# Kernel optimization log

Hardware: AMD Instinct MI355X
Metric: run time of the kernel (lower is better)

## Reference

```python
import jax, jax.numpy as jnp
import numpy as np

NC = 128      # nc
K = 5         # cube kernel size
NS = 3        # n_scale pyramid levels
NV = 150000   # vertices (cortical-surface scale)
NF = 300000   # faces ~ 2*NV
L = 192       # volume side (L = W = H -> rescale = [1,1,1])


def setup_inputs() -> dict:
    key = jax.random.key(0)
    ks = jax.random.split(key, 16)
    s = 0.05
    return {
        "v": jax.random.uniform(ks[0], (1, NV, 3), minval=-0.9, maxval=0.9, dtype=jnp.float32),
        "f": jax.random.randint(ks[1], (1, NF, 3), 0, NV, dtype=jnp.int32),
        "volume": jax.random.normal(ks[2], (1, 1, L, L, L), dtype=jnp.float32),
        "fc1_w": jax.random.normal(ks[3], (6, NC), dtype=jnp.float32) * s,
        "fc1_b": jnp.zeros((NC,), jnp.float32),
        "fc2_w": jax.random.normal(ks[4], (2 * NC, 4 * NC), dtype=jnp.float32) * s,
        "fc2_b": jnp.zeros((4 * NC,), jnp.float32),
        "fc3_w": jax.random.normal(ks[5], (4 * NC, 2 * NC), dtype=jnp.float32) * s,
        "fc3_b": jnp.zeros((2 * NC,), jnp.float32),
        "fc4_w": jax.random.normal(ks[6], (2 * NC, 3), dtype=jnp.float32) * s,
        "fc4_b": jnp.zeros((3,), jnp.float32),
        "conv_w": jax.random.normal(ks[7], (NC, NS, K, K, K), dtype=jnp.float32) * s,
        "conv_b": jnp.zeros((NC,), jnp.float32),
        "lfc_w": jax.random.normal(ks[8], (NC, NC), dtype=jnp.float32) * s,
        "lfc_b": jnp.zeros((NC,), jnp.float32),
    }


def _vertex_normals(v, f):
    # pytorch3d-style vertex normals: scatter-add area-weighted face normals, then normalize.
    verts, faces = v[0], f[0]
    p0, p1, p2 = verts[faces[:, 0]], verts[faces[:, 1]], verts[faces[:, 2]]
    fn = jnp.cross(p1 - p0, p2 - p0)  # [NF, 3]
    n = jnp.zeros_like(verts)
    n = n.at[faces[:, 0]].add(fn).at[faces[:, 1]].add(fn).at[faces[:, 2]].add(fn)
    n = n / jnp.maximum(jnp.linalg.norm(n, axis=-1, keepdims=True), 1e-12)
    return n[None]  # [1, NV, 3]


def _cube_sampling(v, volume):
    # Vectorized version of the 125-iteration Python gather loop:
    # gather a KxKxK neighborhood per vertex at each pyramid scale.
    vol_n = volume[0, 0]
    off = jnp.arange(-(K - 1) // 2, (K - 1) // 2 + 1)  # [-2..2]
    cubes = []
    for n in range(NS):
        if n > 0:
            s = vol_n.shape[0]
            vol_n = vol_n.reshape(s // 2, 2, s // 2, 2, s // 2, 2).mean(axis=(1, 3, 5))  # avg_pool3d(2)
        idx = jnp.round((v[0] + 1.0) * L / 2 ** (n + 1)).astype(jnp.int32)  # rescale = [1,1,1]
        idx = jnp.clip(idx, (K - 1) // 2, L // 2 ** n - 3)
        i0 = idx[:, 0, None, None, None] + off[None, :, None, None]
        i1 = idx[:, 1, None, None, None] + off[None, None, :, None]
        i2 = idx[:, 2, None, None, None] + off[None, None, None, :]
        cubes.append(vol_n[i0, i1, i2])  # [NV, K, K, K]
    return jnp.stack(cubes, axis=1)  # [NV, NS, K, K, K]


def reference(v, f, volume, fc1_w, fc1_b, fc2_w, fc2_b, fc3_w, fc3_b, fc4_w, fc4_b,
              conv_w, conv_b, lfc_w, lfc_b):
    coord = v
    normal = _vertex_normals(v, f)
    x = jnp.concatenate([v, normal], axis=2)                 # [1, NV, 6]
    x = jax.nn.leaky_relu(x @ fc1_w + fc1_b, 0.15)           # [1, NV, NC]
    cubes = _cube_sampling(v, volume)                        # [NV, NS, K, K, K]
    # Conv3d with kernel == input size -> single output voxel == full contraction.
    x_local = jnp.einsum('ncijk,ocijk->no', cubes, conv_w) + conv_b  # [NV, NC]
    x_local = (x_local @ lfc_w + lfc_b)[None]                # [1, NV, NC]
    x = jnp.concatenate([x, x_local], axis=2)                # [1, NV, 2*NC]
    x = jax.nn.leaky_relu(x @ fc2_w + fc2_b, 0.15)
    x = jax.nn.leaky_relu(x @ fc3_w + fc3_b, 0.15)
    x = jnp.tanh(x @ fc4_w + fc4_b) * 0.1
    return coord + x
```

## Files before the change

kernel.cpp:

```cpp
#include <hip/hip_runtime.h>
#include <hip/hip_bf16.h>
#include <math.h>

#define NVERT 150000
#define NFACE 300000
#define LVOL  192
#define TVB   32
#define MTV   48

#define P2_POOL1 3456
#define P2_POOL2 432
#define P2_WC    193
#define P2_CP0   3456
#define P2_POOL2_START (P2_POOL1)
#define P2_WC_START    (P2_POOL1 + P2_POOL2)
#define P2_CP0_START   (P2_POOL1 + P2_POOL2 + P2_WC)

#define NB_NORM 1172
#define NB_TRS  1024

#define NBUCKET 13824
#define WS_BIG_NEED  44808576ull
#define WS_B16_NEED  58964352ull
#define WS_SORT_NEED 60219648ull

typedef short v8s __attribute__((ext_vector_type(8)));
typedef float v4f __attribute__((ext_vector_type(4)));

__device__ __forceinline__ float s2f(short s) {
    unsigned int u = ((unsigned int)(unsigned short)s) << 16;
    return __builtin_bit_cast(float, u);
}
__device__ __forceinline__ short f2s(float f) {
    __hip_bfloat16 h = __float2bfloat16(f);
    return __builtin_bit_cast(short, h);
}
__device__ __forceinline__ float lrelu(float x) { return x > 0.f ? x : 0.15f * x; }

__device__ __forceinline__ float ldf(const void* __restrict__ p, int i, int bf) {
    return bf ? s2f(((const short*)p)[i]) : ((const float*)p)[i];
}

__device__ __forceinline__ int haddr(int r, int c) {
    int hi  = c >> 7;
    int mid = (c >> 4) & 7;
    int lo  = c & 15;
    int wc  = hi * 64 + (mid & 3) * 16 + lo;
    return ((mid < 4) ? 0 : 12672) + r * 264 + wc;
}

__global__ void detect_kernel(const void* __restrict__ v, int* __restrict__ flag) {
    __shared__ int s_ok;
    int t = threadIdx.x;
    if (t == 0) s_ok = 1;
    __syncthreads();
    float x = s2f(((const short*)v)[t]);
    if (!(fabsf(x) <= 1.0f)) atomicAnd(&s_ok, 0);
    __syncthreads();
    if (t == 0) *flag = s_ok;
}

__global__ __launch_bounds__(256) void sort_hist_kernel(
    const void* __restrict__ v, int* __restrict__ hist, int* __restrict__ keys,
    const int* __restrict__ flag)
{
    const int bf = *flag;
    int vert = blockIdx.x * 256 + threadIdx.x;
    if (vert >= NVERT) return;
    float vx = ldf(v, vert * 3 + 0, bf);
    float vy = ldf(v, vert * 3 + 1, bf);
    float vz = ldf(v, vert * 3 + 2, bf);
    int cx = min(max((int)rintf((vx + 1.0f) * 96.0f), 2), 189);
    int cy = min(max((int)rintf((vy + 1.0f) * 96.0f), 2), 189);
    int cz = min(max((int)rintf((vz + 1.0f) * 96.0f), 2), 189);
    int key = ((cx >> 3) * 24 + (cy >> 3)) * 24 + (cz >> 3);
    keys[vert] = key;
    atomicAdd(&hist[key], 1);
}

__global__ __launch_bounds__(1024) void sort_scan_kernel(int* __restrict__ hist)
{
    __shared__ int partial[1024];
    const int t = threadIdx.x;
    const int CH = 14;
    int base = t * CH;
    int sum = 0;
    #pragma unroll
    for (int i = 0; i < CH; i++) {
        int idx = base + i;
        if (idx < NBUCKET) sum += hist[idx];
    }
    partial[t] = sum;
    __syncthreads();
    for (int off = 1; off < 1024; off <<= 1) {
        int x = (t >= off) ? partial[t - off] : 0;
        __syncthreads();
        partial[t] += x;
        __syncthreads();
    }
    int run = partial[t] - sum;
    for (int i = 0; i < CH; i++) {
        int idx = base + i;
        if (idx < NBUCKET) {
            int c = hist[idx];
            hist[idx] = run;
            run += c;
        }
    }
}

__global__ __launch_bounds__(256) void sort_scatter_kernel(
    int* __restrict__ cursor, const int* __restrict__ keys, int* __restrict__ perm)
{
    int vert = blockIdx.x * 256 + threadIdx.x;
    if (vert >= NVERT) return;
    int pos = atomicAdd(&cursor[keys[vert]], 1);
    perm[pos] = vert;
}

__global__ __launch_bounds__(256) void mega_prep2_kernel(
    const void* __restrict__ volume,
    short* __restrict__ vol1b, short* __restrict__ vol2b,
    const void* __restrict__ conv_w, const void* __restrict__ lfc_w,
    const void* __restrict__ conv_b, const void* __restrict__ lfc_b,
    short* __restrict__ Wcomb, float* __restrict__ bcomb,
    const int* __restrict__ flag,
    short* __restrict__ vol0b)
{
    const int bf = *flag;
    const int bid = blockIdx.x;
    const int t = threadIdx.x;

    if (bid < P2_POOL1) {
        int id = bid * 256 + t;
        int z = id % 96, y = (id / 96) % 96, x = id / (96 * 96);
        float s = 0.f;
        #pragma unroll
        for (int a = 0; a < 2; a++)
            #pragma unroll
            for (int b = 0; b < 2; b++)
                #pragma unroll
                for (int c = 0; c < 2; c++)
                    s += ldf(volume, (2 * x + a) * (LVOL * LVOL) + (2 * y + b) * LVOL + (2 * z + c), bf);
        s *= 0.125f;
        vol1b[id] = f2s(s);
    } else if (bid < P2_WC_START) {
        int id = (bid - P2_POOL2_START) * 256 + t;
        int z = id % 48, y = (id / 48) % 48, x = id / (48 * 48);
        float s = 0.f;
        for (int a = 0; a < 4; a++)
            for (int b = 0; b < 4; b++)
                #pragma unroll
                for (int c = 0; c < 4; c++)
                    s += ldf(volume, (4 * x + a) * (LVOL * LVOL) + (4 * y + b) * LVOL + (4 * z + c), bf);
        s *= 0.015625f;
        vol2b[id] = f2s(s);
    } else if (bid < P2_CP0_START) {
        int id = (bid - P2_WC_START) * 256 + t;
        if (id < 49152) {
            int j = id / 384, k = id - j * 384;
            float acc = 0.f;
            if (k < 375) {
                float a0 = 0.f, a1 = 0.f, a2 = 0.f, a3 = 0.f;
                for (int o = 0; o < 128; o += 4) {
                    a0 += ldf(conv_w, (o + 0) * 375 + k, bf) * ldf(lfc_w, (o + 0) * 128 + j, bf);
                    a1 += ldf(conv_w, (o + 1) * 375 + k, bf) * ldf(lfc_w, (o + 1) * 128 + j, bf);
                    a2 += ldf(conv_w, (o + 2) * 375 + k, bf) * ldf(lfc_w, (o + 2) * 128 + j, bf);
                    a3 += ldf(conv_w, (o + 3) * 375 + k, bf) * ldf(lfc_w, (o + 3) * 128 + j, bf);
                }
                acc = (a0 + a1) + (a2 + a3);
            }
            int tile = j >> 4, ln = j & 15;
            int kk = k >> 5, r = k & 31, qq = r >> 3, e = r & 7;
            Wcomb[((tile * 12 + kk) * 64 + qq * 16 + ln) * 8 + e] = f2s(acc);
        } else if (id < 49152 + 128) {
            int j = id - 49152;
            float acc = ldf(lfc_b, j, bf);
            for (int o = 0; o < 128; o++) acc += ldf(conv_b, o, bf) * ldf(lfc_w, o * 128 + j, bf);
            bcomb[j] = acc;
        }
    } else {
        if (bf) return;
        int id = (bid - P2_CP0_START) * 2048 + t * 8;
        const float* vp = (const float*)volume;
        short tmp[8];
        #pragma unroll
        for (int i = 0; i < 8; i++) tmp[i] = f2s(vp[id + i]);
        *(v8s*)&vol0b[id] = *(v8s*)tmp;
    }
}

__global__ __launch_bounds__(256, 6) void gather_ext_kernel(
    const void* __restrict__ v,
    const int* __restrict__ f, float* __restrict__ n_accum,
    const void* __restrict__ volume,
    const short* __restrict__ vol1b,
    const short* __restrict__ vol2b,
    const short* __restrict__ vol0b,
    const int* __restrict__ perm,
    const short* __restrict__ Wcomb,
    const float* __restrict__ bcomb,
    const void* __restrict__ fc2_w, const void* __restrict__ fc3_w,
    short* __restrict__ fc2T, short* __restrict__ fc3T,
    short* __restrict__ xloc,
    const int* __restrict__ flag, int ngather)
{
    __shared__ __align__(16) short sCube[TVB * 392];
    __shared__ int sIdx[TVB * 4];

    const int bf = *flag;
    const int t = threadIdx.x;
    const int bid = blockIdx.x;

    if (bid >= ngather) {
        int rb = bid - ngather;
        if (rb < NB_NORM) {
            int ft = rb * 256 + t;
            if (ft >= NFACE) return;
            int i0 = f[ft * 3 + 0], i1 = f[ft * 3 + 1], i2 = f[ft * 3 + 2];
            float p0x = ldf(v, i0 * 3 + 0, bf), p0y = ldf(v, i0 * 3 + 1, bf), p0z = ldf(v, i0 * 3 + 2, bf);
            float p1x = ldf(v, i1 * 3 + 0, bf), p1y = ldf(v, i1 * 3 + 1, bf), p1z = ldf(v, i1 * 3 + 2, bf);
            float p2x = ldf(v, i2 * 3 + 0, bf), p2y = ldf(v, i2 * 3 + 1, bf), p2z = ldf(v, i2 * 3 + 2, bf);
            float e1x = p1x - p0x, e1y = p1y - p0y, e1z = p1z - p0z;
            float e2x = p2x - p0x, e2y = p2y - p0y, e2z = p2z - p0z;
            float cx = e1y * e2z - e1z * e2y;
            float cy = e1z * e2x - e1x * e2z;
            float cz = e1x * e2y - e1y * e2x;
            atomicAdd(&n_accum[i0 * 3 + 0], cx); atomicAdd(&n_accum[i0 * 3 + 1], cy); atomicAdd(&n_accum[i0 * 3 + 2], cz);
            atomicAdd(&n_accum[i1 * 3 + 0], cx); atomicAdd(&n_accum[i1 * 3 + 1], cy); atomicAdd(&n_accum[i1 * 3 + 2], cz);
            atomicAdd(&n_accum[i2 * 3 + 0], cx); atomicAdd(&n_accum[i2 * 3 + 1], cy); atomicAdd(&n_accum[i2 * 3 + 2], cz);
        } else {
            int id = (rb - NB_NORM) * 256 + t;
            if (id < 131072) {
                int col = id >> 8, k = id & 255;
                int tile = col >> 4, ln = col & 15;
                int kk = k >> 5, r = k & 31, qq = r >> 3, e = r & 7;
                fc2T[((tile * 8 + kk) * 64 + qq * 16 + ln) * 8 + e] = f2s(ldf(fc2_w, k * 512 + col, bf));
            } else {
                int i = id - 131072;
                int col = i >> 9, k = i & 511;
                int tile = col >> 4, ln = col & 15;
                int kk = k >> 5, r = k & 31, qq = r >> 3, e = r & 7;
                fc3T[((tile * 16 + kk) * 64 + qq * 16 + ln) * 8 + e] = f2s(ldf(fc3_w, k * 256 + col, bf));
            }
        }
        return;
    }

    const int base = bid * TVB;
    const int w = t >> 6, L = t & 63, q = L >> 4, ln = L & 15;
    const short* v0 = bf ? (const short*)volume : vol0b;

    if (t < TVB) {
        int slot = min(base + t, NVERT - 1);
        int vert = perm ? perm[slot] : slot;
        float vx = ldf(v, vert * 3 + 0, bf);
        float vy = ldf(v, vert * 3 + 1, bf);
        float vz = ldf(v, vert * 3 + 2, bf);
        #pragma unroll
        for (int n = 0; n < 3; n++) {
            float scl = (n == 0) ? 96.0f : (n == 1 ? 48.0f : 24.0f);
            int dim = LVOL >> n, lim = dim - 3;
            int cx = min(max((int)rintf((vx + 1.0f) * scl), 2), lim);
            int cy = min(max((int)rintf((vy + 1.0f) * scl), 2), lim);
            int cz = min(max((int)rintf((vz + 1.0f) * scl), 2), lim);
            sIdx[t * 4 + n] = (cx * dim + cy) * dim + (cz - 2);
        }
    }
    __syncthreads();

    for (int idx = t; idx < TVB * 75; idx += 256) {
        int n   = idx / 800;
        int rem = idx - n * 800;
        int vl  = rem / 25;
        int dd  = rem - vl * 25;
        int di  = dd / 5, dj = dd - di * 5;
        int dim = LVOL >> n;
        int addr = sIdx[vl * 4 + n] + (di - 2) * dim * dim + (dj - 2) * dim;
        short* dst = &sCube[vl * 392 + n * 125 + dd * 5];
        if (n == 0 && v0 == nullptr) {
            const float* vp = (const float*)volume;
            #pragma unroll
            for (int i = 0; i < 5; i++) dst[i] = f2s(vp[addr + i]);
        } else {
            const short* lvl = (n == 0) ? v0 : (n == 1 ? vol1b : vol2b);
            #pragma unroll
            for (int i = 0; i < 5; i++) dst[i] = lvl[addr + i];
        }
    }
    for (int idx = t; idx < TVB * 9; idx += 256) {
        int vl = idx / 9, rr = idx - vl * 9;
        sCube[vl * 392 + 375 + rr] = 0;
    }
    __syncthreads();

    #pragma unroll
    for (int nt = 0; nt < 2; nt++) {
        int col = w * 32 + nt * 16 + ln;
        const short* wb = Wcomb + ((w * 2 + nt) * 12 * 64 + q * 16 + ln) * 8;
        v4f acc0 = {0.f, 0.f, 0.f, 0.f}, acc1 = {0.f, 0.f, 0.f, 0.f};
        #pragma unroll
        for (int k0 = 0; k0 < 12; k0++) {
            v8s b  = *(const v8s*)(wb + k0 * 512);
            v8s a0 = *(const v8s*)&sCube[ln * 392 + k0 * 32 + q * 8];
            v8s a1 = *(const v8s*)&sCube[(16 + ln) * 392 + k0 * 32 + q * 8];
            acc0 = __builtin_amdgcn_mfma_f32_16x16x32_bf16(a0, b, acc0, 0, 0, 0);
            acc1 = __builtin_amdgcn_mfma_f32_16x16x32_bf16(a1, b, acc1, 0, 0, 0);
        }
        float bias = bcomb[col];
        #pragma unroll
        for (int r = 0; r < 4; r++) {
            xloc[(base + q * 4 + r) * 128 + col]      = f2s(acc0[r] + bias);
            xloc[(base + 16 + q * 4 + r) * 128 + col] = f2s(acc1[r] + bias);
        }
    }
}

__global__ __launch_bounds__(256, 3) void mlp_kernel(
    const void* __restrict__ v,
    const float* __restrict__ n_accum,
    const short* __restrict__ xloc,
    const int* __restrict__ perm,
    const short* __restrict__ fc2T,
    const short* __restrict__ fc3T,
    const void* __restrict__ fc1_w, const void* __restrict__ fc1_b,
    const void* __restrict__ fc2_b, const void* __restrict__ fc3_b,
    const void* __restrict__ fc4_w, const void* __restrict__ fc4_b,
    void* __restrict__ out,
    const int* __restrict__ flag)
{
    __shared__ __align__(16) char smem[52224];
    short* sX  = (short*)smem;
    short* sHB = (short*)smem;
    short* s3  = (short*)smem;
    short* sW4 = (short*)(smem + 50688);

    const int bf = *flag;
    const int t = threadIdx.x;
    const int base = blockIdx.x * MTV;
    const int w = t >> 6, L = t & 63, q = L >> 4, ln = L & 15;
    const int laneoff = (q * 16 + ln) * 8;

    for (int id = t; id < MTV * 16; id += 256) {
        int row = id >> 4, seg = id & 15;
        v8s x = *(const v8s*)(xloc + (base + row) * 128 + seg * 8);
        *(v8s*)&sX[row * 264 + 128 + seg * 8] = x;
    }

    for (int i = t; i < 768; i += 256) {
        int j = i >> 8, k = i & 255;
        sW4[i] = f2s(ldf(fc4_w, k * 3 + j, bf));
    }

    {
        int vi = t >> 2, cb = (t & 3) * 32;
        if (vi < MTV) {
            int vert = perm ? perm[base + vi] : (base + vi);
            float i0 = ldf(v, vert * 3 + 0, bf);
            float i1 = ldf(v, vert * 3 + 1, bf);
            float i2 = ldf(v, vert * 3 + 2, bf);
            float nx = n_accum[vert * 3 + 0];
            float ny = n_accum[vert * 3 + 1];
            float nz = n_accum[vert * 3 + 2];
            float inv = 1.0f / fmaxf(sqrtf(nx * nx + ny * ny + nz * nz), 1e-12f);
            float i3 = nx * inv, i4 = ny * inv, i5 = nz * inv;
            #pragma unroll 8
            for (int i = 0; i < 32; i++) {
                int c = cb + i;
                float acc = ldf(fc1_b, c, bf)
                          + i0 * ldf(fc1_w, 0 * 128 + c, bf)
                          + i1 * ldf(fc1_w, 1 * 128 + c, bf)
                          + i2 * ldf(fc1_w, 2 * 128 + c, bf)
                          + i3 * ldf(fc1_w, 3 * 128 + c, bf)
                          + i4 * ldf(fc1_w, 4 * 128 + c, bf)
                          + i5 * ldf(fc1_w, 5 * 128 + c, bf);
                sX[vi * 264 + c] = f2s(lrelu(acc));
            }
        }
    }
    __syncthreads();

    {
        #pragma unroll
        for (int nt = 4; nt < 8; nt++) {
            int col = w * 128 + nt * 16 + ln;
            const short* bb = fc2T + (w * 8 + nt) * 8 * 512 + laneoff;
            v4f acc0 = {0.f, 0.f, 0.f, 0.f}, acc1 = {0.f, 0.f, 0.f, 0.f}, acc2 = {0.f, 0.f, 0.f, 0.f};
            #pragma unroll
            for (int k0 = 0; k0 < 8; k0++) {
                v8s b  = *(const v8s*)(bb + k0 * 512);
                v8s a0 = *(const v8s*)&sX[(ln) * 264 + k0 * 32 + q * 8];
                v8s a1 = *(const v8s*)&sX[(16 + ln) * 264 + k0 * 32 + q * 8];
                v8s a2 = *(const v8s*)&sX[(32 + ln) * 264 + k0 * 32 + q * 8];
                acc0 = __builtin_amdgcn_mfma_f32_16x16x32_bf16(a0, b, acc0, 0, 0, 0);
                acc1 = __builtin_amdgcn_mfma_f32_16x16x32_bf16(a1, b, acc1, 0, 0, 0);
                acc2 = __builtin_amdgcn_mfma_f32_16x16x32_bf16(a2, b, acc2, 0, 0, 0);
            }
            float bias = ldf(fc2_b, col, bf);
            int wc = 12672 + w * 64 + (nt - 4) * 16 + ln;
            #pragma unroll
            for (int r = 0; r < 4; r++) {
                sHB[(q * 4 + r) * 264 + wc]      = f2s(lrelu(acc0[r] + bias));
                sHB[(16 + q * 4 + r) * 264 + wc] = f2s(lrelu(acc1[r] + bias));
                sHB[(32 + q * 4 + r) * 264 + wc] = f2s(lrelu(acc2[r] + bias));
            }
        }

        v4f accL[4][3];
        #pragma unroll
        for (int nt = 0; nt < 4; nt++)
            #pragma unroll
            for (int m = 0; m < 3; m++)
                accL[nt][m] = (v4f){0.f, 0.f, 0.f, 0.f};

        #pragma unroll
        for (int nt = 0; nt < 4; nt++) {
            const short* bb = fc2T + (w * 8 + nt) * 8 * 512 + laneoff;
            #pragma unroll
            for (int k0 = 0; k0 < 8; k0++) {
                v8s b  = *(const v8s*)(bb + k0 * 512);
                v8s a0 = *(const v8s*)&sX[(ln) * 264 + k0 * 32 + q * 8];
                v8s a1 = *(const v8s*)&sX[(16 + ln) * 264 + k0 * 32 + q * 8];
                v8s a2 = *(const v8s*)&sX[(32 + ln) * 264 + k0 * 32 + q * 8];
                accL[nt][0] = __builtin_amdgcn_mfma_f32_16x16x32_bf16(a0, b, accL[nt][0], 0, 0, 0);
                accL[nt][1] = __builtin_amdgcn_mfma_f32_16x16x32_bf16(a1, b, accL[nt][1], 0, 0, 0);
                accL[nt][2] = __builtin_amdgcn_mfma_f32_16x16x32_bf16(a2, b, accL[nt][2], 0, 0, 0);
            }
        }
        __syncthreads();

        #pragma unroll
        for (int nt = 0; nt < 4; nt++) {
            int col = w * 128 + nt * 16 + ln;
            float bias = ldf(fc2_b, col, bf);
            int wc = w * 64 + nt * 16 + ln;
            #pragma unroll
            for (int r = 0; r < 4; r++) {
                sHB[(q * 4 + r) * 264 + wc]      = f2s(lrelu(accL[nt][0][r] + bias));
                sHB[(16 + q * 4 + r) * 264 + wc] = f2s(lrelu(accL[nt][1][r] + bias));
                sHB[(32 + q * 4 + r) * 264 + wc] = f2s(lrelu(accL[nt][2][r] + bias));
            }
        }
    }
    __syncthreads();

    {
        v4f acc[4][3];
        #pragma unroll
        for (int nt = 0; nt < 4; nt++)
            #pragma unroll
            for (int m = 0; m < 3; m++)
                acc[nt][m] = (v4f){0.f, 0.f, 0.f, 0.f};

        #pragma unroll
        for (int half = 0; half < 2; half++) {
            v8s A0[8], A1[8], A2[8];
            #pragma unroll
            for (int k0 = 0; k0 < 8; k0++) {
                int c = half * 256 + k0 * 32 + q * 8;
                A0[k0] = *(const v8s*)&sHB[haddr(ln, c)];
                A1[k0] = *(const v8s*)&sHB[haddr(16 + ln, c)];
                A2[k0] = *(const v8s*)&sHB[haddr(32 + ln, c)];
            }
            #pragma unroll
            for (int nt = 0; nt < 4; nt++) {
                const short* bb = fc3T + ((w * 4 + nt) * 16 + half * 8) * 512 + laneoff;
                v8s B[8];
                #pragma unroll
                for (int k0 = 0; k0 < 8; k0++) B[k0] = *(const v8s*)(bb + k0 * 512);
                #pragma unroll
                for (int k0 = 0; k0 < 8; k0++) {
                    acc[nt][0] = __builtin_amdgcn_mfma_f32_16x16x32_bf16(A0[k0], B[k0], acc[nt][0], 0, 0, 0);
                    acc[nt][1] = __builtin_amdgcn_mfma_f32_16x16x32_bf16(A1[k0], B[k0], acc[nt][1], 0, 0, 0);
                    acc[nt][2] = __builtin_amdgcn_mfma_f32_16x16x32_bf16(A2[k0], B[k0], acc[nt][2], 0, 0, 0);
                }
            }
        }
        __syncthreads();

        #pragma unroll
        for (int nt = 0; nt < 4; nt++) {
            int col = w * 64 + nt * 16 + ln;
            float bias = ldf(fc3_b, col, bf);
            #pragma unroll
            for (int r = 0; r < 4; r++) {
                s3[(q * 4 + r) * 264 + col]      = f2s(lrelu(acc[nt][0][r] + bias));
                s3[(16 + q * 4 + r) * 264 + col] = f2s(lrelu(acc[nt][1][r] + bias));
                s3[(32 + q * 4 + r) * 264 + col] = f2s(lrelu(acc[nt][2][r] + bias));
            }
        }
    }
    __syncthreads();

    {
        int vi = t >> 2, l = t & 3;
        if (vi < MTV) {
            float p0 = 0.f, p1 = 0.f, p2 = 0.f;
            for (int k = l * 8; k < 256; k += 32) {
                #pragma unroll
                for (int j = 0; j < 8; j++) {
                    float a = s2f(s3[vi * 264 + k + j]);
                    p0 += a * s2f(sW4[0 * 256 + k + j]);
                    p1 += a * s2f(sW4[1 * 256 + k + j]);
                    p2 += a * s2f(sW4[2 * 256 + k + j]);
                }
            }
            #pragma unroll
            for (int s = 2; s; s >>= 1) {
                p0 += __shfl_down(p0, s, 4);
                p1 += __shfl_down(p1, s, 4);
                p2 += __shfl_down(p2, s, 4);
            }
            if (l == 0) {
                int vert = perm ? perm[base + vi] : (base + vi);
                float vx = ldf(v, vert * 3 + 0, bf);
                float vy = ldf(v, vert * 3 + 1, bf);
                float vz = ldf(v, vert * 3 + 2, bf);
                float o0 = vx + 0.1f * tanhf(p0 + ldf(fc4_b, 0, bf));
                float o1 = vy + 0.1f * tanhf(p1 + ldf(fc4_b, 1, bf));
                float o2 = vz + 0.1f * tanhf(p2 + ldf(fc4_b, 2, bf));
                if (bf) {
                    short* ob = (short*)out;
                    ob[vert * 3 + 0] = f2s(o0);
                    ob[vert * 3 + 1] = f2s(o1);
                    ob[vert * 3 + 2] = f2s(o2);
                } else {
                    float* of = (float*)out;
                    of[vert * 3 + 0] = o0;
                    of[vert * 3 + 1] = o1;
                    of[vert * 3 + 2] = o2;
                }
            }
        }
    }
}

__global__ __launch_bounds__(256, 3) void fused_mfma_kernel(
    const void* __restrict__ v,
    const float* __restrict__ n_accum,
    const void* __restrict__ volume,
    const short* __restrict__ vol1,
    const short* __restrict__ vol2,
    const short* __restrict__ Wcomb,
    const float* __restrict__ bcomb,
    const short* __restrict__ fc2T,
    const short* __restrict__ fc3T,
    const void* __restrict__ fc1_w, const void* __restrict__ fc1_b,
    const void* __restrict__ fc2_b, const void* __restrict__ fc3_b,
    const void* __restrict__ fc4_w, const void* __restrict__ fc4_b,
    void* __restrict__ out,
    const int* __restrict__ flag)
{
    __shared__ __align__(16) char smem[51712];
    short* sX    = (short*)smem;
    short* sCube = (short*)(smem + 16896);
    short* sH    = (short*)(smem + 16896);
    short* s3    = (short*)smem;
    short* sW4   = (short*)(smem + 50176);

    const int bf = *flag;
    const int t = threadIdx.x;
    const int base = blockIdx.x * TVB;
    const int w = t >> 6, L = t & 63, q = L >> 4, ln = L & 15;
    const int laneoff = (q * 16 + ln) * 8;

    for (int idx = t; idx < TVB * 75; idx += 256) {
        int vl  = idx / 75;
        int r75 = idx - vl * 75;
        int n   = r75 / 25;
        int dd  = r75 - n * 25;
        int di  = dd / 5, dj = dd - di * 5;
        int vert = base + vl;
        short* dst = &sCube[vl * 392 + n * 125 + dd * 5];
        if (vert < NVERT) {
            float vx = ldf(v, vert * 3 + 0, bf);
            float vy = ldf(v, vert * 3 + 1, bf);
            float vz = ldf(v, vert * 3 + 2, bf);
            float scl = (n == 0) ? 96.0f : (n == 1 ? 48.0f : 24.0f);
            int lim = (LVOL >> n) - 3;
            int cx = (int)rintf((vx + 1.0f) * scl);
            int cy = (int)rintf((vy + 1.0f) * scl);
            int cz = (int)rintf((vz + 1.0f) * scl);
            cx = min(max(cx, 2), lim) + di - 2;
            cy = min(max(cy, 2), lim) + dj - 2;
            cz = min(max(cz, 2), lim);
            if (n == 0) {
                int b0 = (cx * LVOL + cy) * LVOL + (cz - 2);
                if (bf) {
                    const short* vp = (const short*)volume;
                    #pragma unroll
                    for (int i = 0; i < 5; i++) dst[i] = vp[b0 + i];
                } else {
                    const float* vp = (const float*)volume;
                    #pragma unroll
                    for (int i = 0; i < 5; i++) dst[i] = f2s(vp[b0 + i]);
                }
            } else {
                const short* lvl = (n == 1) ? vol1 : vol2;
                int dim = (n == 1) ? 96 : 48;
                int b0 = (cx * dim + cy) * dim + (cz - 2);
                #pragma unroll
                for (int i = 0; i < 5; i++) dst[i] = lvl[b0 + i];
            }
        } else {
            #pragma unroll
            for (int i = 0; i < 5; i++) dst[i] = 0;
        }
    }
    for (int idx = t; idx < TVB * 9; idx += 256) {
        int vl = idx / 9, rr = idx - vl * 9;
        sCube[vl * 392 + 375 + rr] = 0;
    }
    for (int i = t; i < 768; i += 256) {
        int j = i >> 8, k = i & 255;
        sW4[i] = f2s(ldf(fc4_w, k * 3 + j, bf));
    }
    {
        int vi = t & 31, cb = (t >> 5) * 16;
        int vert = base + vi;
        float i0 = 0.f, i1 = 0.f, i2 = 0.f, i3 = 0.f, i4 = 0.f, i5 = 0.f;
        if (vert < NVERT) {
            i0 = ldf(v, vert * 3 + 0, bf);
            i1 = ldf(v, vert * 3 + 1, bf);
            i2 = ldf(v, vert * 3 + 2, bf);
            float nx = n_accum[vert * 3 + 0];
            float ny = n_accum[vert * 3 + 1];
            float nz = n_accum[vert * 3 + 2];
            float inv = 1.0f / fmaxf(sqrtf(nx * nx + ny * ny + nz * nz), 1e-12f);
            i3 = nx * inv; i4 = ny * inv; i5 = nz * inv;
        }
        #pragma unroll
        for (int i = 0; i < 16; i++) {
            int c = cb + i;
            float acc = ldf(fc1_b, c, bf)
                      + i0 * ldf(fc1_w, 0 * 128 + c, bf)
                      + i1 * ldf(fc1_w, 1 * 128 + c, bf)
                      + i2 * ldf(fc1_w, 2 * 128 + c, bf)
                      + i3 * ldf(fc1_w, 3 * 128 + c, bf)
                      + i4 * ldf(fc1_w, 4 * 128 + c, bf)
                      + i5 * ldf(fc1_w, 5 * 128 + c, bf);
            sX[vi * 264 + c] = f2s(lrelu(acc));
        }
    }
    __syncthreads();

    #pragma unroll
    for (int nt = 0; nt < 2; nt++) {
        int col = w * 32 + nt * 16 + ln;
        const short* wb = Wcomb + ((w * 2 + nt) * 12 * 64) * 8 + laneoff;
        v4f acc0 = {0.f, 0.f, 0.f, 0.f}, acc1 = {0.f, 0.f, 0.f, 0.f};
        #pragma unroll
        for (int k0 = 0; k0 < 12; k0++) {
            v8s b  = *(const v8s*)(wb + k0 * 512);
            v8s a0 = *(const v8s*)&sCube[ln * 392 + k0 * 32 + q * 8];
            v8s a1 = *(const v8s*)&sCube[(16 + ln) * 392 + k0 * 32 + q * 8];
            acc0 = __builtin_amdgcn_mfma_f32_16x16x32_bf16(a0, b, acc0, 0, 0, 0);
            acc1 = __builtin_amdgcn_mfma_f32_16x16x32_bf16(a1, b, acc1, 0, 0, 0);
        }
        float bias = bcomb[col];
        #pragma unroll
        for (int r = 0; r < 4; r++) {
            sX[(q * 4 + r) * 264 + 128 + col]      = f2s(acc0[r] + bias);
            sX[(16 + q * 4 + r) * 264 + 128 + col] = f2s(acc1[r] + bias);
        }
    }
    __syncthreads();

    {
        v8s a0[8], a1[8];
        #pragma unroll
        for (int k0 = 0; k0 < 8; k0++) {
            a0[k0] = *(const v8s*)&sX[ln * 264 + k0 * 32 + q * 8];
            a1[k0] = *(const v8s*)&sX[(16 + ln) * 264 + k0 * 32 + q * 8];
        }
        #pragma unroll
        for (int nt = 0; nt < 8; nt++) {
            int col = w * 128 + nt * 16 + ln;
            const short* bb = fc2T + (w * 8 + nt) * 8 * 512 + laneoff;
            v4f acc0 = {0.f, 0.f, 0.f, 0.f}, acc1 = {0.f, 0.f, 0.f, 0.f};
            #pragma unroll
            for (int k0 = 0; k0 < 8; k0++) {
                v8s b = *(const v8s*)(bb + k0 * 512);
                acc0 = __builtin_amdgcn_mfma_f32_16x16x32_bf16(a0[k0], b, acc0, 0, 0, 0);
                acc1 = __builtin_amdgcn_mfma_f32_16x16x32_bf16(a1[k0], b, acc1, 0, 0, 0);
            }
            float bias = ldf(fc2_b, col, bf);
            #pragma unroll
            for (int r = 0; r < 4; r++) {
                sH[(q * 4 + r) * 520 + col]      = f2s(lrelu(acc0[r] + bias));
                sH[(16 + q * 4 + r) * 520 + col] = f2s(lrelu(acc1[r] + bias));
            }
        }
    }
    __syncthreads();

    {
        #pragma unroll
        for (int nt = 0; nt < 4; nt++) {
            int col = w * 64 + nt * 16 + ln;
            v4f acc0 = {0.f, 0.f, 0.f, 0.f}, acc1 = {0.f, 0.f, 0.f, 0.f};
            #pragma unroll
            for (int half = 0; half < 2; half++) {
                const short* bb = fc3T + ((w * 4 + nt) * 16 + half * 8) * 512 + laneoff;
                #pragma unroll
                for (int k0 = 0; k0 < 8; k0++) {
                    v8s b  = *(const v8s*)(bb + k0 * 512);
                    v8s a0 = *(const v8s*)&sH[ln * 520 + half * 256 + k0 * 32 + q * 8];
                    v8s a1 = *(const v8s*)&sH[(16 + ln) * 520 + half * 256 + k0 * 32 + q * 8];
                    acc0 = __builtin_amdgcn_mfma_f32_16x16x32_bf16(a0, b, acc0, 0, 0, 0);
                    acc1 = __builtin_amdgcn_mfma_f32_16x16x32_bf16(a1, b, acc1, 0, 0, 0);
                }
            }
            float bias = ldf(fc3_b, col, bf);
            #pragma unroll
            for (int r = 0; r < 4; r++) {
                s3[(q * 4 + r) * 264 + col]      = f2s(lrelu(acc0[r] + bias));
                s3[(16 + q * 4 + r) * 264 + col] = f2s(lrelu(acc1[r] + bias));
            }
        }
    }
    __syncthreads();

    {
        int vi = t >> 3, l = t & 7;
        float p0 = 0.f, p1 = 0.f, p2 = 0.f;
        for (int k = l; k < 256; k += 8) {
            float a = s2f(s3[vi * 264 + k]);
            p0 += a * s2f(sW4[0 * 256 + k]);
            p1 += a * s2f(sW4[1 * 256 + k]);
            p2 += a * s2f(sW4[2 * 256 + k]);
        }
        #pragma unroll
        for (int s = 4; s; s >>= 1) {
            p0 += __shfl_down(p0, s, 8);
            p1 += __shfl_down(p1, s, 8);
            p2 += __shfl_down(p2, s, 8);
        }
        if (l == 0) {
            int vert = base + vi;
            if (vert < NVERT) {
                float vx = ldf(v, vert * 3 + 0, bf);
                float vy = ldf(v, vert * 3 + 1, bf);
                float vz = ldf(v, vert * 3 + 2, bf);
                float o0 = vx + 0.1f * tanhf(p0 + ldf(fc4_b, 0, bf));
                float o1 = vy + 0.1f * tanhf(p1 + ldf(fc4_b, 1, bf));
                float o2 = vz + 0.1f * tanhf(p2 + ldf(fc4_b, 2, bf));
                if (bf) {
                    short* ob = (short*)out;
                    ob[vert * 3 + 0] = f2s(o0);
                    ob[vert * 3 + 1] = f2s(o1);
                    ob[vert * 3 + 2] = f2s(o2);
                } else {
                    float* of = (float*)out;
                    of[vert * 3 + 0] = o0;
                    of[vert * 3 + 1] = o1;
                    of[vert * 3 + 2] = o2;
                }
            }
        }
    }
}

extern "C" void kernel_launch(void* const* d_in, const int* in_sizes, int n_in,
                              void* d_out, int out_size, void* d_ws, size_t ws_size,
                              hipStream_t stream) {
    const void* v      = d_in[0];
    const int*  f      = (const int*)d_in[1];
    const void* volume = d_in[2];
    const void* fc1_w  = d_in[3];
    const void* fc1_b  = d_in[4];
    const void* fc2_w  = d_in[5];
    const void* fc2_b  = d_in[6];
    const void* fc3_w  = d_in[7];
    const void* fc3_b  = d_in[8];
    const void* fc4_w  = d_in[9];
    const void* fc4_b  = d_in[10];
    const void* conv_w = d_in[11];
    const void* conv_b = d_in[12];
    const void* lfc_w  = d_in[13];
    const void* lfc_b  = d_in[14];

    char* wsb = (char*)d_ws;
    const int big  = (ws_size >= WS_BIG_NEED) ? 1 : 0;
    const int b16  = (ws_size >= WS_B16_NEED) ? 1 : 0;
    const int srt  = (ws_size >= WS_SORT_NEED) ? 1 : 0;

    if (big) {
        int*   flag    = (int*)wsb;
        float* n_accum = (float*)(wsb + 64);
        short* vol1b   = (short*)(wsb + 1800064);
        short* vol2b   = (short*)(wsb + 5339008);
        short* Wcomb   = (short*)(wsb + 5781376);
        float* bcomb   = (float*)(wsb + 5879680);
        short* fc2T    = (short*)(wsb + 5880192);
        short* fc3T    = (short*)(wsb + 6142336);
        short* xloc    = (short*)(wsb + 6404480);
        short* vol0b   = b16 ? (short*)(wsb + 44808576) : nullptr;
        int*   hist    = srt ? (int*)(wsb + 58964352) : nullptr;
        int*   keys    = srt ? (int*)(wsb + 59019648) : nullptr;
        int*   perm    = srt ? (int*)(wsb + 59619648) : nullptr;

        hipMemsetAsync(n_accum, 0, NVERT * 3 * sizeof(float), stream);
        detect_kernel<<<1, 256, 0, stream>>>(v, flag);
        if (srt) {
            hipMemsetAsync(hist, 0, NBUCKET * sizeof(int), stream);
            sort_hist_kernel<<<(NVERT + 255) / 256, 256, 0, stream>>>(v, hist, keys, flag);
            sort_scan_kernel<<<1, 1024, 0, stream>>>(hist);
            sort_scatter_kernel<<<(NVERT + 255) / 256, 256, 0, stream>>>(hist, keys, perm);
        }
        mega_prep2_kernel<<<P2_CP0_START + (b16 ? P2_CP0 : 0), 256, 0, stream>>>(
            volume, vol1b, vol2b,
            conv_w, lfc_w, conv_b, lfc_b, Wcomb, bcomb, flag, vol0b);
        int ngather = (NVERT + TVB - 1) / TVB;
        gather_ext_kernel<<<ngather + NB_NORM + NB_TRS, 256, 0, stream>>>(
            v, f, n_accum, volume, vol1b, vol2b, vol0b, perm, Wcomb, bcomb,
            fc2_w, fc3_w, fc2T, fc3T, xloc, flag, ngather);
        mlp_kernel<<<(NVERT + MTV - 1) / MTV, 256, 0, stream>>>(
            v, n_accum, xloc, perm, fc2T, fc3T,
            fc1_w, fc1_b, fc2_b, fc3_b, fc4_w, fc4_b, d_out, flag);
    } else {
        int*   flag    = (int*)wsb;
        float* n_accum = (float*)(wsb + 64);
        short* vol1    = (short*)(wsb + 1800064);
        short* vol2    = (short*)(wsb + 3569536);
        short* Wcomb   = (short*)(wsb + 3790720);
        float* bcomb   = (float*)(wsb + 3889024);
        short* fc2T    = (short*)(wsb + 3889536);
        short* fc3T    = (short*)(wsb + 4151680);

        hipMemsetAsync(n_accum, 0, NVERT * 3 * sizeof(float), stream);
        detect_kernel<<<1, 256, 0, stream>>>(v, flag);
        mega_prep2_kernel<<<P2_CP0_START, 256, 0, stream>>>(
            volume, vol1, vol2,
            conv_w, lfc_w, conv_b, lfc_b, Wcomb, bcomb, flag, nullptr);
        gather_ext_kernel<<<NB_NORM + NB_TRS, 256, 0, stream>>>(
            v, f, n_accum, volume, vol1, vol2, nullptr, nullptr, Wcomb, bcomb,
            fc2_w, fc3_w, fc2T, fc3T, nullptr, flag, 0);
        fused_mfma_kernel<<<(NVERT + TVB - 1) / TVB, 256, 0, stream>>>(
            v, n_accum, volume, vol1, vol2, Wcomb, bcomb, fc2T, fc3T,
            fc1_w, fc1_b, fc2_b, fc3_b, fc4_w, fc4_b, d_out, flag);
    }
}
```

Baseline: 556.2 us.

## Add padded 8-wide row cube gather kernel with matching combined weight layout

Adds a new gather kernel that loads each 5-voxel row of the cube neighbourhood as one aligned 16-byte chunk (three dwords plus shifting for odd alignment) into shared memory, padding the contraction dimension from 375 to 608. A second combined conv/lfc weight buffer in the matching padded layout is built in the prep kernel. The aim is to replace per-element gathers with wide vector loads and simpler indexing. The cost is about 60% more MFMA work per vertex from the zero padding, larger shared memory that lowers occupancy, and extra prep blocks.

```diff
diff --git a/kernel.cpp b/kernel.cpp
--- a/kernel.cpp
+++ b/kernel.cpp
@@ -11,10 +11,12 @@
 #define P2_POOL1 3456
 #define P2_POOL2 432
 #define P2_WC    193
+#define P2_WC8   304
 #define P2_CP0   3456
 #define P2_POOL2_START (P2_POOL1)
 #define P2_WC_START    (P2_POOL1 + P2_POOL2)
-#define P2_CP0_START   (P2_POOL1 + P2_POOL2 + P2_WC)
+#define P2_WC8_START   (P2_WC_START + P2_WC)
+#define P2_CP0_START   (P2_WC8_START + P2_WC8)
 
 #define NB_NORM 1172
 #define NB_TRS  1024
@@ -26,6 +28,7 @@
 
 typedef short v8s __attribute__((ext_vector_type(8)));
 typedef float v4f __attribute__((ext_vector_type(4)));
+typedef unsigned int v4u __attribute__((ext_vector_type(4)));
 
 __device__ __forceinline__ float s2f(short s) {
     unsigned int u = ((unsigned int)(unsigned short)s) << 16;
@@ -123,7 +126,7 @@
     short* __restrict__ vol1b, short* __restrict__ vol2b,
     const void* __restrict__ conv_w, const void* __restrict__ lfc_w,
     const void* __restrict__ conv_b, const void* __restrict__ lfc_b,
-    short* __restrict__ Wcomb, float* __restrict__ bcomb,
+    short* __restrict__ Wcomb, short* __restrict__ Wcomb8, float* __restrict__ bcomb,
     const int* __restrict__ flag,
     short* __restrict__ vol0b)
 {
@@ -155,7 +158,7 @@
                     s += ldf(volume, (4 * x + a) * (LVOL * LVOL) + (4 * y + b) * LVOL + (4 * z + c), bf);
         s *= 0.015625f;
         vol2b[id] = f2s(s);
-    } else if (bid < P2_CP0_START) {
+    } else if (bid < P2_WC8_START) {
         int id = (bid - P2_WC_START) * 256 + t;
         if (id < 49152) {
             int j = id / 384, k = id - j * 384;
@@ -179,6 +182,25 @@
             for (int o = 0; o < 128; o++) acc += ldf(conv_b, o, bf) * ldf(lfc_w, o * 128 + j, bf);
             bcomb[j] = acc;
         }
+    } else if (bid < P2_CP0_START) {
+        int id = (bid - P2_WC8_START) * 256 + t;
+        int j = id / 608, k = id - j * 608;
+        int r = k >> 3, e = k & 7;
+        float acc = 0.f;
+        if (e < 5 && r < 75) {
+            int k375 = (r / 25) * 125 + (r % 25) * 5 + e;
+            float a0 = 0.f, a1 = 0.f, a2 = 0.f, a3 = 0.f;
+            for (int o = 0; o < 128; o += 4) {
+                a0 += ldf(conv_w, (o + 0) * 375 + k375, bf) * ldf(lfc_w, (o + 0) * 128 + j, bf);
+                a1 += ldf(conv_w, (o + 1) * 375 + k375, bf) * ldf(lfc_w, (o + 1) * 128 + j, bf);
+                a2 += ldf(conv_w, (o + 2) * 375 + k375, bf) * ldf(lfc_w, (o + 2) * 128 + j, bf);
+                a3 += ldf(conv_w, (o + 3) * 375 + k375, bf) * ldf(lfc_w, (o + 3) * 128 + j, bf);
+            }
+            acc = (a0 + a1) + (a2 + a3);
+        }
+        int tile = j >> 4, ln = j & 15;
+        int kk = k >> 5, rr = k & 31, qq = rr >> 3, ee = rr & 7;
+        Wcomb8[((tile * 19 + kk) * 64 + qq * 16 + ln) * 8 + ee] = f2s(acc);
     } else {
         if (bf) return;
         int id = (bid - P2_CP0_START) * 2048 + t * 8;
@@ -187,6 +209,144 @@
         #pragma unroll
         for (int i = 0; i < 8; i++) tmp[i] = f2s(vp[id + i]);
         *(v8s*)&vol0b[id] = *(v8s*)tmp;
+    }
+}
+
+__global__ __launch_bounds__(256, 4) void gather8_kernel(
+    const void* __restrict__ v,
+    const int* __restrict__ f, float* __restrict__ n_accum,
+    const void* __restrict__ volume,
+    const short* __restrict__ vol1b,
+    const short* __restrict__ vol2b,
+    const short* __restrict__ vol0b,
+    const int* __restrict__ perm,
+    const short* __restrict__ Wcomb8,
+    const float* __restrict__ bcomb,
+    const void* __restrict__ fc2_w, const void* __restrict__ fc3_w,
+    short* __restrict__ fc2T, short* __restrict__ fc3T,
+    short* __restrict__ xloc,
+    const int* __restrict__ flag, int ngather)
+{
+    __shared__ __align__(16) short sCube[TVB * 608];
+    __shared__ int sIdx[TVB * 4];
+
+    const int bf = *flag;
+    const int t = threadIdx.x;
+    const int bid = blockIdx.x;
+
+    if (bid >= ngather) {
+        int rb = bid - ngather;
+        if (rb < NB_NORM) {
+            int ft = rb * 256 + t;
+            if (ft >= NFACE) return;
+            int i0 = f[ft * 3 + 0], i1 = f[ft * 3 + 1], i2 = f[ft * 3 + 2];
+            float p0x = ldf(v, i0 * 3 + 0, bf), p0y = ldf(v, i0 * 3 + 1, bf), p0z = ldf(v, i0 * 3 + 2, bf);
+            float p1x = ldf(v, i1 * 3 + 0, bf), p1y = ldf(v, i1 * 3 + 1, bf), p1z = ldf(v, i1 * 3 + 2, bf);
+            float p2x = ldf(v, i2 * 3 + 0, bf), p2y = ldf(v, i2 * 3 + 1, bf), p2z = ldf(v, i2 * 3 + 2, bf);
+            float e1x = p1x - p0x, e1y = p1y - p0y, e1z = p1z - p0z;
+            float e2x = p2x - p0x, e2y = p2y - p0y, e2z = p2z - p0z;
+            float cx = e1y * e2z - e1z * e2y;
+            float cy = e1z * e2x - e1x * e2z;
+            float cz = e1x * e2y - e1y * e2x;
+            atomicAdd(&n_accum[i0 * 3 + 0], cx); atomicAdd(&n_accum[i0 * 3 + 1], cy); atomicAdd(&n_accum[i0 * 3 + 2], cz);
+            atomicAdd(&n_accum[i1 * 3 + 0], cx); atomicAdd(&n_accum[i1 * 3 + 1], cy); atomicAdd(&n_accum[i1 * 3 + 2], cz);
+            atomicAdd(&n_accum[i2 * 3 + 0], cx); atomicAdd(&n_accum[i2 * 3 + 1], cy); atomicAdd(&n_accum[i2 * 3 + 2], cz);
+        } else {
+            int id = (rb - NB_NORM) * 256 + t;
+            if (id < 131072) {
+                int col = id >> 8, k = id & 255;
+                int tile = col >> 4, ln = col & 15;
+                int kk = k >> 5, r = k & 31, qq = r >> 3, e = r & 7;
+                fc2T[((tile * 8 + kk) * 64 + qq * 16 + ln) * 8 + e] = f2s(ldf(fc2_w, k * 512 + col, bf));
+            } else {
+                int i = id - 131072;
+                int col = i >> 9, k = i & 511;
+                int tile = col >> 4, ln = col & 15;
+                int kk = k >> 5, r = k & 31, qq = r >> 3, e = r & 7;
+                fc3T[((tile * 16 + kk) * 64 + qq * 16 + ln) * 8 + e] = f2s(ldf(fc3_w, k * 256 + col, bf));
+            }
+        }
+        return;
+    }
+
+    const int base = bid * TVB;
+    const int w = t >> 6, L = t & 63, q = L >> 4, ln = L & 15;
+    const short* v0 = bf ? (const short*)volume : vol0b;
+
+    if (t < TVB) {
+        int slot = min(base + t, NVERT - 1);
+        int vert = perm ? perm[slot] : slot;
+        float vx = ldf(v, vert * 3 + 0, bf);
+        float vy = ldf(v, vert * 3 + 1, bf);
+        float vz = ldf(v, vert * 3 + 2, bf);
+        #pragma unroll
+        for (int n = 0; n < 3; n++) {
+            float scl = (n == 0) ? 96.0f : (n == 1 ? 48.0f : 24.0f);
+            int dim = LVOL >> n, lim = dim - 3;
+            int cx = min(max((int)rintf((vx + 1.0f) * scl), 2), lim);
+            int cy = min(max((int)rintf((vy + 1.0f) * scl), 2), lim);
+            int cz = min(max((int)rintf((vz + 1.0f) * scl), 2), lim);
+            sIdx[t * 4 + n] = (cx * dim + cy) * dim + (cz - 2);
+        }
+        *(v4u*)&sCube[t * 608 + 600] = (v4u){0u, 0u, 0u, 0u};
+    }
+    __syncthreads();
+
+    for (int idx = t; idx < TVB * 75; idx += 256) {
+        int n   = idx / 800;
+        int rem = idx - n * 800;
+        int vl  = rem / 25;
+        int dd  = rem - vl * 25;
+        int di  = dd / 5, dj = dd - di * 5;
+        int dim = LVOL >> n;
+        int addr = sIdx[vl * 4 + n] + (di - 2) * dim * dim + (dj - 2) * dim;
+        int r = n * 25 + dd;
+        if (n == 0 && bf) {
+            const short* vp = (const short*)volume;
+            short* dst = &sCube[vl * 608 + r * 8];
+            #pragma unroll
+            for (int i = 0; i < 5; i++) dst[i] = vp[addr + i];
+            dst[5] = 0; dst[6] = 0; dst[7] = 0;
+        } else {
+            const short* lvl = (n == 0) ? v0 : (n == 1 ? vol1b : vol2b);
+            int p  = addr & 1;
+            int a0 = addr - p;
+            const unsigned int* u = (const unsigned int*)(lvl + a0);
+            unsigned int x0 = u[0], x1 = u[1], x2 = u[2];
+            unsigned int d0, d1, d2;
+            if (p) {
+                d0 = (x0 >> 16) | (x1 << 16);
+                d1 = (x1 >> 16) | (x2 << 16);
+                d2 = (x2 >> 16);
+            } else {
+                d0 = x0;
+                d1 = x1;
+                d2 = x2 & 0xFFFFu;
+            }
+            *(v4u*)&sCube[vl * 608 + r * 8] = (v4u){d0, d1, d2, 0u};
+        }
+    }
+    __syncthreads();
+
+    #pragma unroll
+    for (int nt = 0; nt < 2; nt++) {
+        int col = w * 32 + nt * 16 + ln;
+        const short* wb = Wcomb8 + ((w * 2 + nt) * 19 * 64 + q * 16 + ln) * 8;
+        v4f acc0 = {0.f, 0.f, 0.f, 0.f}, acc1 = {0.f, 0.f, 0.f, 0.f};
+        #pragma unroll
+        for (int k0 = 0; k0 < 19; k0++) {
+            v8s b  = *(const v8s*)(wb + k0 * 512);
+            v8s a0 = *(const v8s*)&sCube[ln * 608 + k0 * 32 + q * 8];
+            v8s a1 = *(const v8s*)&sCube[(16 + ln) * 608 + k0 * 32 + q * 8];
+            acc0 = __builtin_amdgcn_mfma_f32_16x16x32_bf16(a0, b, acc0, 0, 0, 0);
+            acc1 = __builtin_amdgcn_mfma_f32_16x16x32_bf16(a1, b, acc1, 0, 0, 0);
+        }
+        float bias = bcomb[col];
+        #pragma unroll
+        for (int r = 0; r < 4; r++) {
+            xloc[(base + q * 4 + r) * 128 + col]      = f2s(acc0[r] + bias);
+            xloc[(base + 16 + q * 4 + r) * 128 + col] = f2s(acc1[r] + bias);
+        }
     }
 }
 
@@ -790,6 +950,7 @@
         float* n_accum = (float*)(wsb + 64);
         short* vol1b   = (short*)(wsb + 1800064);
         short* vol2b   = (short*)(wsb + 5339008);
+        short* Wcomb8  = (short*)(wsb + 5560192);
         short* Wcomb   = (short*)(wsb + 5781376);
         float* bcomb   = (float*)(wsb + 5879680);
         short* fc2T    = (short*)(wsb + 5880192);
@@ -810,11 +971,17 @@
         }
         mega_prep2_kernel<<<P2_CP0_START + (b16 ? P2_CP0 : 0), 256, 0, stream>>>(
             volume, vol1b, vol2b,
-            conv_w, lfc_w, conv_b, lfc_b, Wcomb, bcomb, flag, vol0b);
+            conv_w, lfc_w, conv_b, lfc_b, Wcomb, Wcomb8, bcomb, flag, vol0b);
         int ngather = (NVERT + TVB - 1) / TVB;
-        gather_ext_kernel<<<ngather + NB_NORM + NB_TRS, 256, 0, stream>>>(
-            v, f, n_accum, volume, vol1b, vol2b, vol0b, perm, Wcomb, bcomb,
-            fc2_w, fc3_w, fc2T, fc3T, xloc, flag, ngather);
+        if (srt) {
+            gather8_kernel<<<ngather + NB_NORM + NB_TRS, 256, 0, stream>>>(
+                v, f, n_accum, volume, vol1b, vol2b, vol0b, perm, Wcomb8, bcomb,
+                fc2_w, fc3_w, fc2T, fc3T, xloc, flag, ngather);
+        } else {
+            gather_ext_kernel<<<ngather + NB_NORM + NB_TRS, 256, 0, stream>>>(
+                v, f, n_accum, volume, vol1b, vol2b, vol0b, nullptr, Wcomb, bcomb,
+                fc2_w, fc3_w, fc2T, fc3T, xloc, flag, ngather);
+        }
         mlp_kernel<<<(NVERT + MTV - 1) / MTV, 256, 0, stream>>>(
             v, n_accum, xloc, perm, fc2T, fc3T,
             fc1_w, fc1_b, fc2_b, fc3_b, fc4_w, fc4_b, d_out, flag);
@@ -830,9 +997,9 @@
 
         hipMemsetAsync(n_accum, 0, NVERT * 3 * sizeof(float), stream);
         detect_kernel<<<1, 256, 0, stream>>>(v, flag);
-        mega_prep2_kernel<<<P2_CP0_START, 256, 0, stream>>>(
+        mega_prep2_kernel<<<P2_WC8_START, 256, 0, stream>>>(
             volume, vol1, vol2,
-            conv_w, lfc_w, conv_b, lfc_b, Wcomb, bcomb, flag, nullptr);
+            conv_w, lfc_w, conv_b, lfc_b, Wcomb, nullptr, bcomb, flag, nullptr);
         gather_ext_kernel<<<NB_NORM + NB_TRS, 256, 0, stream>>>(
             v, f, n_accum, volume, vol1, vol2, nullptr, nullptr, Wcomb, bcomb,
             fc2_w, fc3_w, fc2T, fc3T, nullptr, flag, 0);
```

Measured after the change: 550.6 us. Within noise of the previous version (-1.0%).
